# Kernel tuning notes

Hardware: AMD Instinct MI355X
Metric: run time of the kernel (lower is better)

## Reference

```python
import jax, jax.numpy as jnp
import numpy as np

MAX_SENTENCE = 12
HIDDEN = 256
INPUT = 18 * 300
NEG = -9999999.0


def _lstm(xs, Wih, Whh, bih, bhh):
    # xs: [T, B, I] -> hs: [T, B, H] (torch LSTM gate order i,f,g,o)
    B = xs.shape[1]
    H = Whh.shape[1]

    def step(carry, x):
        h, c = carry
        g = x @ Wih.T + h @ Whh.T + bih + bhh
        i, f, gg, o = jnp.split(g, 4, axis=-1)
        c = jax.nn.sigmoid(f) * c + jax.nn.sigmoid(i) * jnp.tanh(gg)
        h = jax.nn.sigmoid(o) * jnp.tanh(c)
        return (h, c), h

    init = (jnp.zeros((B, H), xs.dtype), jnp.zeros((B, H), xs.dtype))
    _, hs = jax.lax.scan(step, init, xs)
    return hs


def setup_inputs() -> dict:
    key = jax.random.key(0)
    ks = jax.random.split(key, 16)
    s = 0.05
    return {
        "x": jax.random.normal(ks[0], (512, MAX_SENTENCE, INPUT), jnp.float32),
        "Wih_f": jax.random.normal(ks[1], (4 * HIDDEN, INPUT), jnp.float32) * s,
        "Whh_f": jax.random.normal(ks[2], (4 * HIDDEN, HIDDEN), jnp.float32) * s,
        "bih_f": jax.random.normal(ks[3], (4 * HIDDEN,), jnp.float32) * s,
        "bhh_f": jax.random.normal(ks[4], (4 * HIDDEN,), jnp.float32) * s,
        "Wih_b": jax.random.normal(ks[5], (4 * HIDDEN, INPUT), jnp.float32) * s,
        "Whh_b": jax.random.normal(ks[6], (4 * HIDDEN, HIDDEN), jnp.float32) * s,
        "bih_b": jax.random.normal(ks[7], (4 * HIDDEN,), jnp.float32) * s,
        "bhh_b": jax.random.normal(ks[8], (4 * HIDDEN,), jnp.float32) * s,
        "enc_W": jax.random.normal(ks[9], (50, 2 * HIDDEN), jnp.float32) * s,
        "enc_b": jax.random.normal(ks[10], (50,), jnp.float32) * s,
        "wfc_W": jax.random.normal(ks[11], (1, 100), jnp.float32) * s,
        "wfc_b": jax.random.normal(ks[12], (1,), jnp.float32) * s,
        "fc_W": jax.random.normal(ks[13], (2, MAX_SENTENCE), jnp.float32) * s,
        "fc_b": jax.random.normal(ks[14], (2,), jnp.float32) * s,
    }


def reference(x, Wih_f, Whh_f, bih_f, bhh_f, Wih_b, Whh_b, bih_b, bhh_b,
              enc_W, enc_b, wfc_W, wfc_b, fc_W, fc_b):
    # Bidirectional LSTM over the document axis (seq-first, batch = MAX_SENTENCE)
    hf = _lstm(x, Wih_f, Whh_f, bih_f, bhh_f)                       # [D, S, H]
    hb = jnp.flip(_lstm(jnp.flip(x, 0), Wih_b, Whh_b, bih_b, bhh_b), 0)
    H = jnp.concatenate([hf, hb], axis=-1)                           # [D, S, 2H]

    # Sentence encoder: Linear(2H,50) + LeakyReLU (dropout = identity, eval)
    enc = jax.nn.leaky_relu(H @ enc_W.T + enc_b, 0.01)               # [D, S, 50]

    # Pairwise affinity Wij[d,i,j] = w_fc(concat(enc_i, enc_j)); split-weight trick
    w1, w2 = wfc_W[0, :50], wfc_W[0, 50:]
    a = enc @ w1                                                     # [D, S]
    b = enc @ w2                                                     # [D, S]
    Wij = a[:, :, None] + b[:, None, :] + wfc_b[0]                   # [D, S, S]
    eye = jnp.eye(MAX_SENTENCE, dtype=bool)
    Wij = jnp.where(eye, NEG, Wij)

    # Core sentence: argmax over off-diagonal row sums
    rowsum = jnp.sum(jnp.where(eye, 0.0, Wij), axis=-1)              # [D, S]
    core = jnp.argmax(rowsum, axis=-1)                               # [D]

    # Cosine similarity of each sentence to the core sentence -> rank scores
    Hn = H / (jnp.linalg.norm(H, axis=-1, keepdims=True) + 1e-12)
    core_vec = jnp.take_along_axis(Hn, core[:, None, None], axis=1)  # [D, 1, 2H]
    sim = jnp.sum(Hn * core_vec, axis=-1)                            # [D, S]
    order = jnp.argsort(-sim, axis=-1)
    ranks = jnp.argsort(order, axis=-1)
    rank_score = 1.0 - ranks.astype(H.dtype) / MAX_SENTENCE          # [D, S]

    # Row-scaled affinities, zero diagonal for aggregation
    Wmask = jnp.where(eye, 0.0, Wij) * rank_score[:, :, None]        # [D, S, S]

    # Two rounds of weighted neighbor aggregation
    emb = H
    for _ in range(2):
        emb = emb + jnp.einsum('dij,djh->dih', Wmask, emb)

    doc = jnp.mean(emb, axis=-1)                                     # [D, S]
    return doc @ fc_W.T + fc_b                                       # [D, 2]
```

## Files before the change

kernel.cpp:

```cpp
#include <hip/hip_runtime.h>
#include <hip/hip_bf16.h>
#include <hip/hip_fp16.h>


typedef _Float16 h8 __attribute__((ext_vector_type(8)));
typedef _Float16 h2 __attribute__((ext_vector_type(2)));
typedef float f4 __attribute__((ext_vector_type(4)));

#define SEQ 512
#define NL 12
#define KIN 5400
#define KP 5408
#define NG 2048
#define MROWS 6144

__device__ __forceinline__ unsigned int pk2(float a, float b){
  h2 v; v[0] = (_Float16)a; v[1] = (_Float16)b;
  return __builtin_bit_cast(unsigned int, v);
}
__device__ __forceinline__ float dot2u(unsigned int h, unsigned int w, float acc){
  return __builtin_amdgcn_fdot2(__builtin_bit_cast(h2, h), __builtin_bit_cast(h2, w), acc, false);
}
__device__ __forceinline__ float sigm(float x){ return 1.f/(1.f + __expf(-x)); }
__device__ __forceinline__ float tanhx(float x){ return 1.f - 2.f/(__expf(2.f*x) + 1.f); }

__global__ void cvt_x(const float* __restrict__ x, _Float16* __restrict__ xh){
  int idx = blockIdx.x * 256 + threadIdx.x;
  int row = idx / KP, col = idx - row * KP;
  float v = (col < KIN) ? x[(size_t)row * KIN + col] : 0.f;
  xh[idx] = (_Float16)v;
}

__global__ void cvt_w(const float* __restrict__ wf, const float* __restrict__ wb,
                      _Float16* __restrict__ wh){
  int idx = blockIdx.x * 256 + threadIdx.x;
  int row = idx / KP, col = idx - row * KP;
  float v = 0.f;
  if (col < KIN)
    v = (row < 1024) ? wf[(size_t)row * KIN + col] : wb[(size_t)(row - 1024) * KIN + col];
  wh[idx] = (_Float16)v;
}

__global__ __launch_bounds__(256) void gemm_in(
    const _Float16* __restrict__ A, const _Float16* __restrict__ B, _Float16* __restrict__ G,
    const float* __restrict__ bif, const float* __restrict__ bhf,
    const float* __restrict__ bib, const float* __restrict__ bhb){
  __shared__ _Float16 As[128 * 40];
  __shared__ _Float16 Bs[128 * 40];
  int tid = threadIdx.x;
  int bm = blockIdx.x % 48, bn = blockIdx.x / 48;
  int wid = tid >> 6, ln = tid & 63;
  int wm = wid & 1, wn = wid >> 1;
  int l15 = ln & 15, q = ln >> 4;
  int i0 = tid, i1 = tid + 256;
  int r0 = i0 >> 2, c0 = i0 & 3, r1 = i1 >> 2, c1 = i1 & 3;
  const size_t a0 = (size_t)(bm*128 + r0) * KP + c0*8;
  const size_t a1 = (size_t)(bm*128 + r1) * KP + c1*8;
  const size_t b0 = (size_t)(bn*128 + r0) * KP + c0*8;
  const size_t b1 = (size_t)(bn*128 + r1) * KP + c1*8;
  f4 acc[4][4] = {};
  for (int kk = 0; kk < 169; ++kk){
    int k0 = kk * 32;
    uint4 va0 = *(const uint4*)(A + a0 + k0);
    uint4 va1 = *(const uint4*)(A + a1 + k0);
    uint4 vb0 = *(const uint4*)(B + b0 + k0);
    uint4 vb1 = *(const uint4*)(B + b1 + k0);
    __syncthreads();
    *(uint4*)(As + r0*40 + c0*8) = va0;
    *(uint4*)(As + r1*40 + c1*8) = va1;
    *(uint4*)(Bs + r0*40 + c0*8) = vb0;
    *(uint4*)(Bs + r1*40 + c1*8) = vb1;
    __syncthreads();
    h8 af[4], bfr[4];
    #pragma unroll
    for (int mt = 0; mt < 4; ++mt)
      af[mt] = *(const h8*)(As + (wm*64 + mt*16 + l15)*40 + q*8);
    #pragma unroll
    for (int nt = 0; nt < 4; ++nt)
      bfr[nt] = *(const h8*)(Bs + (wn*64 + nt*16 + l15)*40 + q*8);
    #pragma unroll
    for (int mt = 0; mt < 4; ++mt)
      #pragma unroll
      for (int nt = 0; nt < 4; ++nt)
        acc[mt][nt] = __builtin_amdgcn_mfma_f32_16x16x32_f16(af[mt], bfr[nt], acc[mt][nt], 0, 0, 0);
  }
  float bias[4];
  #pragma unroll
  for (int nt = 0; nt < 4; ++nt){
    int col = bn*128 + wn*64 + nt*16 + l15;
    bias[nt] = (col < 1024) ? (bif[col] + bhf[col]) : (bib[col-1024] + bhb[col-1024]);
  }
  #pragma unroll
  for (int mt = 0; mt < 4; ++mt)
    #pragma unroll
    for (int nt = 0; nt < 4; ++nt)
      #pragma unroll
      for (int r = 0; r < 4; ++r){
        int row = bm*128 + wm*64 + mt*16 + q*4 + r;
        int col = bn*128 + wn*64 + nt*16 + l15;
        G[(size_t)row * NG + col] = (_Float16)(acc[mt][nt][r] + bias[nt]);
      }
}

__global__ __launch_bounds__(512, 2) void lstm_rec(
    const float* __restrict__ Whhf, const float* __restrict__ Whhb,
    const _Float16* __restrict__ G, float* __restrict__ Hout){
  __shared__ unsigned int tailw[12][1024];
  __shared__ unsigned int hlds[128];
  __shared__ float fg[256], og[256];
  int b = blockIdx.x;
  int dir = b / 12, lane = b - dir * 12;
  int t = threadIdx.x;
  const float* Whh = dir ? Whhb : Whhf;
  int r0 = t, r1 = t + 512;
  unsigned int wa[116], wb[116];
  #pragma unroll
  for (int c = 0; c < 128; ++c){
    float2 v0 = *(const float2*)(Whh + (size_t)r0 * 256 + 2*c);
    float2 v1 = *(const float2*)(Whh + (size_t)r1 * 256 + 2*c);
    unsigned int u0 = pk2(v0.x, v0.y);
    unsigned int u1 = pk2(v1.x, v1.y);
    if (c < 116){ wa[c] = u0; wb[c] = u1; }
    else { tailw[c - 116][r0] = u0; tailw[c - 116][r1] = u1; }
  }
  if (t < 128) hlds[t] = 0u;
  float cst = 0.f;
  __syncthreads();
  for (int it = 0; it < SEQ; ++it){
    int s = dir ? (SEQ - 1 - it) : it;
    const _Float16* gp = G + (size_t)(s*NL + lane) * NG + dir * 1024;
    float ga = (float)gp[r0];
    float gb = (float)gp[r1];
    float acc0 = 0.f, acc1 = 0.f;
    #pragma unroll
    for (int c4 = 0; c4 < 29; ++c4){
      uint4 hq = *(const uint4*)&hlds[c4*4];
      unsigned int ha[4] = {hq.x, hq.y, hq.z, hq.w};
      #pragma unroll
      for (int j = 0; j < 4; ++j){
        acc0 = dot2u(ha[j], wa[c4*4 + j], acc0);
        acc1 = dot2u(ha[j], wb[c4*4 + j], acc1);
      }
    }
    #pragma unroll
    for (int c4 = 0; c4 < 3; ++c4){
      uint4 hq = *(const uint4*)&hlds[116 + c4*4];
      unsigned int ha[4] = {hq.x, hq.y, hq.z, hq.w};
      #pragma unroll
      for (int j = 0; j < 4; ++j){
        int cc = c4*4 + j;
        acc0 = dot2u(ha[j], tailw[cc][r0], acc0);
        acc1 = dot2u(ha[j], tailw[cc][r1], acc1);
      }
    }
    acc0 += ga; acc1 += gb;
    __syncthreads();
    if (t >= 256){ fg[t - 256] = acc0; og[t - 256] = acc1; }
    __syncthreads();
    if (t < 256){
      float iv = acc0, gv = acc1, fv = fg[t], ov = og[t];
      cst = sigm(fv)*cst + sigm(iv)*tanhx(gv);
      float hv = sigm(ov)*tanhx(cst);
      ((_Float16*)hlds)[t] = (_Float16)hv;
      Hout[(size_t)(s*NL + lane)*512 + dir*256 + t] = hv;
    }
    __syncthreads();
  }
}

__global__ __launch_bounds__(256) void epilogue(
    const float* __restrict__ H, const float* __restrict__ encW, const float* __restrict__ encB,
    const float* __restrict__ wfcW, const float* __restrict__ wfcB,
    const float* __restrict__ fcW, const float* __restrict__ fcB, float* __restrict__ out){
  __shared__ float B0[12][516];
  __shared__ float B1[12][516];
  __shared__ float encl[12][52];
  __shared__ float part[12][16];
  __shared__ float av[12], bv[12], nrm[12], simv[12], rsv[12], docv[12];
  __shared__ float Wm[12][12];
  __shared__ int corei;
  int d = blockIdx.x, t = threadIdx.x;
  const float* Hd = H + (size_t)d * NL * 512;
  for (int idx = t; idx < NL * 128; idx += 256){
    int i = idx >> 7, h4 = (idx & 127) * 4;
    *(f4*)(&B0[i][h4]) = *(const f4*)(Hd + i*512 + h4);
  }
  __syncthreads();
  for (int idx = t; idx < 600; idx += 256){
    int i = idx % 12, e = idx / 12;
    float s = encB[e];
    const float* w = encW + e * 512;
    for (int h = 0; h < 512; ++h) s += B0[i][h] * w[h];
    encl[i][e] = (s >= 0.f) ? s : 0.01f * s;
  }
  __syncthreads();
  if (t < 12){
    float sa = 0.f, sb = 0.f;
    for (int e = 0; e < 50; ++e){ sa += encl[t][e]*wfcW[e]; sb += encl[t][e]*wfcW[50 + e]; }
    av[t] = sa; bv[t] = sb;
  }
  __syncthreads();
  if (t < 192){
    int i = t >> 4, sl = t & 15;
    float s = 0.f;
    for (int h = sl*32; h < sl*32 + 32; ++h){ float v = B0[i][h]; s += v*v; }
    part[i][sl] = s;
  }
  if (t == 192){
    float wbv = wfcB[0];
    float best = -1e30f; int bi = 0;
    for (int i = 0; i < 12; ++i){
      float rs = 0.f;
      for (int j = 0; j < 12; ++j) if (j != i) rs += av[i] + bv[j] + wbv;
      if (rs > best){ best = rs; bi = i; }
    }
    corei = bi;
  }
  __syncthreads();
  if (t < 12){
    float s = 0.f; for (int l = 0; l < 16; ++l) s += part[t][l];
    nrm[t] = sqrtf(s) + 1e-12f;
  }
  __syncthreads();
  if (t < 192){
    int i = t >> 4, sl = t & 15, cc = corei;
    float s = 0.f;
    for (int h = sl*32; h < sl*32 + 32; ++h) s += B0[i][h] * B0[cc][h];
    part[i][sl] = s;
  }
  __syncthreads();
  if (t < 12){
    float s = 0.f; for (int l = 0; l < 16; ++l) s += part[t][l];
    simv[t] = s / (nrm[t] * nrm[corei]);
  }
  __syncthreads();
  if (t < 12){
    int rk = 0; float st = simv[t];
    for (int j = 0; j < 12; ++j){
      float sj = simv[j];
      rk += (sj > st) || (sj == st && j < t);
    }
    rsv[t] = 1.f - (float)rk / 12.f;
  }
  __syncthreads();
  if (t < 144){
    int i = t / 12, j = t - (t / 12) * 12;
    Wm[i][j] = (i == j) ? 0.f : (av[i] + bv[j] + wfcB[0]) * rsv[i];
  }
  __syncthreads();
  for (int h = t; h < 512; h += 256){
    float e[12];
    #pragma unroll
    for (int j = 0; j < 12; ++j) e[j] = B0[j][h];
    #pragma unroll
    for (int i = 0; i < 12; ++i){
      float s = e[i];
      #pragma unroll
      for (int j = 0; j < 12; ++j) s += Wm[i][j] * e[j];
      B1[i][h] = s;
    }
  }
  __syncthreads();
  for (int h = t; h < 512; h += 256){
    float e[12];
    #pragma unroll
    for (int j = 0; j < 12; ++j) e[j] = B1[j][h];
    #pragma unroll
    for (int i = 0; i < 12; ++i){
      float s = e[i];
      #pragma unroll
      for (int j = 0; j < 12; ++j) s += Wm[i][j] * e[j];
      B0[i][h] = s;
    }
  }
  __syncthreads();
  if (t < 192){
    int i = t >> 4, sl = t & 15;
    float s = 0.f;
    for (int h = sl*32; h < sl*32 + 32; ++h) s += B0[i][h];
    part[i][sl] = s;
  }
  __syncthreads();
  if (t < 12){
    float s = 0.f; for (int l = 0; l < 16; ++l) s += part[t][l];
    docv[t] = s / 512.f;
  }
  __syncthreads();
  if (t < 2){
    float s = fcB[t];
    for (int i = 0; i < 12; ++i) s += docv[i] * fcW[t*12 + i];
    out[d*2 + t] = s;
  }
}

extern "C" void kernel_launch(void* const* d_in, const int* in_sizes, int n_in,
                              void* d_out, int out_size, void* d_ws, size_t ws_size,
                              hipStream_t stream){
  const float* x    = (const float*)d_in[0];
  const float* Wihf = (const float*)d_in[1];
  const float* Whhf = (const float*)d_in[2];
  const float* bihf = (const float*)d_in[3];
  const float* bhhf = (const float*)d_in[4];
  const float* Wihb = (const float*)d_in[5];
  const float* Whhb = (const float*)d_in[6];
  const float* bihb = (const float*)d_in[7];
  const float* bhhb = (const float*)d_in[8];
  const float* encW = (const float*)d_in[9];
  const float* encB = (const float*)d_in[10];
  const float* wfcW = (const float*)d_in[11];
  const float* wfcB = (const float*)d_in[12];
  const float* fcW  = (const float*)d_in[13];
  const float* fcB  = (const float*)d_in[14];
  float* out = (float*)d_out;
  char* ws = (char*)d_ws;
  _Float16* xh = (_Float16*)(ws);
  _Float16* wh = (_Float16*)(ws + 66453504);
  _Float16* G  = (_Float16*)(ws + 88604672);
  float* H = (float*)(ws);

  cvt_x<<<129792, 256, 0, stream>>>(x, xh);
  cvt_w<<<43264, 256, 0, stream>>>(Wihf, Wihb, wh);
  gemm_in<<<768, 256, 0, stream>>>(xh, wh, G, bihf, bhhf, bihb, bhhb);
  lstm_rec<<<24, 512, 0, stream>>>(Whhf, Whhb, G, H);
  epilogue<<<512, 256, 0, stream>>>(H, encW, encB, wfcW, wfcB, fcW, fcB, out);
}
```

Before: 1.657 ms.

## Restructure LSTM recurrence: quad-split K with DPP reduction and double-buffered h

The recurrent kernel now uses 1024 threads per block. Each group of four lanes owns one hidden unit and computes all four gates over a quarter of the K dimension, then combines the partial sums with DPP cross-lane adds. This removes the fg/og shared-memory exchange and two of the three barriers per timestep. The hidden state is double-buffered in LDS, and all of Whh is held in registers, so the LDS-resident tail weights are no longer needed. The costs are a 4x replicated gate computation per unit and a heavier register requirement at 1024 threads.

```diff
diff --git a/kernel.cpp b/kernel.cpp
--- a/kernel.cpp
+++ b/kernel.cpp
@@ -12,7 +12,6 @@
 #define KIN 5400
 #define KP 5408
 #define NG 2048
-#define MROWS 6144
 
 __device__ __forceinline__ unsigned int pk2(float a, float b){
   h2 v; v[0] = (_Float16)a; v[1] = (_Float16)b;
@@ -23,6 +22,14 @@
 }
 __device__ __forceinline__ float sigm(float x){ return 1.f/(1.f + __expf(-x)); }
 __device__ __forceinline__ float tanhx(float x){ return 1.f - 2.f/(__expf(2.f*x) + 1.f); }
+__device__ __forceinline__ float dppadd_b1(float v){
+  int x = __builtin_amdgcn_mov_dpp(__builtin_bit_cast(int, v), 0xB1, 0xF, 0xF, true);
+  return v + __builtin_bit_cast(float, x);
+}
+__device__ __forceinline__ float dppadd_4e(float v){
+  int x = __builtin_amdgcn_mov_dpp(__builtin_bit_cast(int, v), 0x4E, 0xF, 0xF, true);
+  return v + __builtin_bit_cast(float, x);
+}
 
 __global__ void cvt_x(const float* __restrict__ x, _Float16* __restrict__ xh){
   int idx = blockIdx.x * 256 + threadIdx.x;
@@ -102,68 +109,71 @@
       }
 }
 
-__global__ __launch_bounds__(512, 2) void lstm_rec(
+__global__ __launch_bounds__(1024, 4) void lstm_rec(
     const float* __restrict__ Whhf, const float* __restrict__ Whhb,
     const _Float16* __restrict__ G, float* __restrict__ Hout){
-  __shared__ unsigned int tailw[12][1024];
-  __shared__ unsigned int hlds[128];
-  __shared__ float fg[256], og[256];
+  __shared__ _Float16 hlds[2][4][72];
   int b = blockIdx.x;
   int dir = b / 12, lane = b - dir * 12;
   int t = threadIdx.x;
+  int e = t >> 2, q = t & 3;
   const float* Whh = dir ? Whhb : Whhf;
-  int r0 = t, r1 = t + 512;
-  unsigned int wa[116], wb[116];
+
+  uint4 wreg[4][8];
   #pragma unroll
-  for (int c = 0; c < 128; ++c){
-    float2 v0 = *(const float2*)(Whh + (size_t)r0 * 256 + 2*c);
-    float2 v1 = *(const float2*)(Whh + (size_t)r1 * 256 + 2*c);
-    unsigned int u0 = pk2(v0.x, v0.y);
-    unsigned int u1 = pk2(v1.x, v1.y);
-    if (c < 116){ wa[c] = u0; wb[c] = u1; }
-    else { tailw[c - 116][r0] = u0; tailw[c - 116][r1] = u1; }
-  }
-  if (t < 128) hlds[t] = 0u;
+  for (int g = 0; g < 4; ++g){
+    const float* wr = Whh + (size_t)(g*256 + e) * 256 + q*64;
+    #pragma unroll
+    for (int i = 0; i < 8; ++i){
+      f4 v0 = *(const f4*)(wr + i*8);
+      f4 v1 = *(const f4*)(wr + i*8 + 4);
+      wreg[g][i].x = pk2(v0[0], v0[1]);
+      wreg[g][i].y = pk2(v0[2], v0[3]);
+      wreg[g][i].z = pk2(v1[0], v1[1]);
+      wreg[g][i].w = pk2(v1[2], v1[3]);
+    }
+  }
+  if (t < 288) ((unsigned int*)hlds)[t] = 0u;
+
+  const uint4* hq0 = (const uint4*)&hlds[0][q][0];
+  const uint4* hq1 = (const uint4*)&hlds[1][q][0];
+  int s0 = dir ? (SEQ - 1) : 0;
+  long sstep = dir ? -(long)(NL*NG) : (long)(NL*NG);
+  long hstep = dir ? -(long)(NL*512) : (long)(NL*512);
+  const _Float16* gp = G + (size_t)(s0*NL + lane) * NG + dir * 1024 + e;
+  float* hp = Hout + (size_t)(s0*NL + lane) * 512 + dir * 256 + e;
   float cst = 0.f;
   __syncthreads();
+
   for (int it = 0; it < SEQ; ++it){
-    int s = dir ? (SEQ - 1 - it) : it;
-    const _Float16* gp = G + (size_t)(s*NL + lane) * NG + dir * 1024;
-    float ga = (float)gp[r0];
-    float gb = (float)gp[r1];
-    float acc0 = 0.f, acc1 = 0.f;
-    #pragma unroll
-    for (int c4 = 0; c4 < 29; ++c4){
-      uint4 hq = *(const uint4*)&hlds[c4*4];
-      unsigned int ha[4] = {hq.x, hq.y, hq.z, hq.w};
-      #pragma unroll
-      for (int j = 0; j < 4; ++j){
-        acc0 = dot2u(ha[j], wa[c4*4 + j], acc0);
-        acc1 = dot2u(ha[j], wb[c4*4 + j], acc1);
-      }
-    }
-    #pragma unroll
-    for (int c4 = 0; c4 < 3; ++c4){
-      uint4 hq = *(const uint4*)&hlds[116 + c4*4];
-      unsigned int ha[4] = {hq.x, hq.y, hq.z, hq.w};
-      #pragma unroll
-      for (int j = 0; j < 4; ++j){
-        int cc = c4*4 + j;
-        acc0 = dot2u(ha[j], tailw[cc][r0], acc0);
-        acc1 = dot2u(ha[j], tailw[cc][r1], acc1);
-      }
-    }
-    acc0 += ga; acc1 += gb;
-    __syncthreads();
-    if (t >= 256){ fg[t - 256] = acc0; og[t - 256] = acc1; }
-    __syncthreads();
-    if (t < 256){
-      float iv = acc0, gv = acc1, fv = fg[t], ov = og[t];
-      cst = sigm(fv)*cst + sigm(iv)*tanhx(gv);
-      float hv = sigm(ov)*tanhx(cst);
-      ((_Float16*)hlds)[t] = (_Float16)hv;
-      Hout[(size_t)(s*NL + lane)*512 + dir*256 + t] = hv;
-    }
+    float ga = (float)gp[0];
+    float gf = (float)gp[256];
+    float gg = (float)gp[512];
+    float go = (float)gp[768];
+    const uint4* hp16 = (it & 1) ? hq1 : hq0;
+    float a0 = 0.f, a1 = 0.f, a2 = 0.f, a3 = 0.f;
+    #pragma unroll
+    for (int i = 0; i < 8; ++i){
+      uint4 hv = hp16[i];
+      a0 = dot2u(hv.x, wreg[0][i].x, a0); a0 = dot2u(hv.y, wreg[0][i].y, a0);
+      a0 = dot2u(hv.z, wreg[0][i].z, a0); a0 = dot2u(hv.w, wreg[0][i].w, a0);
+      a1 = dot2u(hv.x, wreg[1][i].x, a1); a1 = dot2u(hv.y, wreg[1][i].y, a1);
+      a1 = dot2u(hv.z, wreg[1][i].z, a1); a1 = dot2u(hv.w, wreg[1][i].w, a1);
+      a2 = dot2u(hv.x, wreg[2][i].x, a2); a2 = dot2u(hv.y, wreg[2][i].y, a2);
+      a2 = dot2u(hv.z, wreg[2][i].z, a2); a2 = dot2u(hv.w, wreg[2][i].w, a2);
+      a3 = dot2u(hv.x, wreg[3][i].x, a3); a3 = dot2u(hv.y, wreg[3][i].y, a3);
+      a3 = dot2u(hv.z, wreg[3][i].z, a3); a3 = dot2u(hv.w, wreg[3][i].w, a3);
+    }
+    a0 = dppadd_4e(dppadd_b1(a0));
+    a1 = dppadd_4e(dppadd_b1(a1));
+    a2 = dppadd_4e(dppadd_b1(a2));
+    a3 = dppadd_4e(dppadd_b1(a3));
+    float pi = a0 + ga, pf = a1 + gf, pg = a2 + gg, po = a3 + go;
+    cst = sigm(pf)*cst + sigm(pi)*tanhx(pg);
+    float hv = sigm(po)*tanhx(cst);
+    hlds[(it & 1) ^ 1][e >> 6][e & 63] = (_Float16)hv;
+    if (q == 0) *hp = hv;
+    gp += sstep; hp += hstep;
     __syncthreads();
   }
 }
@@ -321,6 +331,6 @@
   cvt_x<<<129792, 256, 0, stream>>>(x, xh);
   cvt_w<<<43264, 256, 0, stream>>>(Wihf, Wihb, wh);
   gemm_in<<<768, 256, 0, stream>>>(xh, wh, G, bihf, bhhf, bihb, bhhb);
-  lstm_rec<<<24, 512, 0, stream>>>(Whhf, Whhb, G, H);
+  lstm_rec<<<24, 1024, 0, stream>>>(Whhf, Whhb, G, H);
   epilogue<<<512, 256, 0, stream>>>(H, encW, encB, wfcW, wfcB, fcW, fcB, out);
 }
```

Measured after the change: 2.279 ms. +37.6%, slower.
